# Performance work log

Measured on AMD Instinct MI355X. Metric: run time of the kernel, lower is better.

The kernel has to match this reference:

```python
import jax, jax.numpy as jnp
import numpy as np

# dims: d_model D, d_inner DI=2*D, d_state S, dt_rank R, conv kernel K, layers NL
D, DI, S, R, K, NL = 512, 1024, 16, 32, 4, 6
B, L = 4, 1024
EPS = 1e-5


def _ln(x, w, b):
    m = x.mean(-1, keepdims=True)
    v = ((x - m) ** 2).mean(-1, keepdims=True)
    return (x - m) * jax.lax.rsqrt(v + EPS) * w + b


def _causal_conv(x, w, b):
    # depthwise causal conv1d: x [B,L,DI], w [DI,K], left-pad K-1 (matches Conv1d(padding=K-1) then crop)
    xp = jnp.pad(x, ((0, 0), (K - 1, 0), (0, 0)))
    y = sum(xp[:, k:k + x.shape[1], :] * w[:, k] for k in range(K))
    return y + b


def _mamba(h, in_w, cw, cb, xp_w, dt_w, dt_b, A_log, Dp, out_w):
    # h: [B,L,D]
    xz = jnp.einsum('bld,ed->ble', h, in_w)        # [B,L,2*DI]
    x, z = jnp.split(xz, 2, axis=-1)
    x = jax.nn.silu(_causal_conv(x, cw, cb))       # [B,L,DI]
    dbc = jnp.einsum('bld,ed->ble', x, xp_w)       # [B,L,R+2S]
    dt_r, Bm, Cm = dbc[..., :R], dbc[..., R:R + S], dbc[..., R + S:]
    dt = jax.nn.softplus(jnp.einsum('blr,dr->bld', dt_r, dt_w) + dt_b)  # [B,L,DI]
    A = -jnp.exp(A_log)                            # [DI,S]

    def step(hst, inp):
        dt_t, B_t, C_t, x_t = inp                  # [B,DI],[B,S],[B,S],[B,DI]
        dA = jnp.exp(dt_t[..., None] * A)          # [B,DI,S]
        hst = dA * hst + (dt_t * x_t)[..., None] * B_t[:, None, :]
        y = jnp.einsum('bds,bs->bd', hst, C_t)
        return hst, y

    h0 = jnp.zeros((x.shape[0], DI, S), x.dtype)
    xs = (dt.transpose(1, 0, 2), Bm.transpose(1, 0, 2), Cm.transpose(1, 0, 2), x.transpose(1, 0, 2))
    _, ys = jax.lax.scan(step, h0, xs)
    y = ys.transpose(1, 0, 2) + x * Dp
    y = y * jax.nn.silu(z)
    return jnp.einsum('bld,ed->ble', y, out_w)     # [B,L,D]


def setup_inputs() -> dict:
    key = jax.random.key(0)
    ks = jax.random.split(key, 10)
    n = lambda k, shp, s: s * jax.random.normal(k, shp, jnp.float32)
    inp = {}
    inp['xs_pad'] = jax.random.normal(ks[0], (B, L, D), jnp.float32)
    inp['ilens'] = jax.random.randint(ks[1], (B,), 1, L + 1)
    inp['norm_w'] = jnp.ones((NL, D), jnp.float32)
    inp['norm_b'] = jnp.zeros((NL, D), jnp.float32)
    inp['in_proj_w'] = n(ks[2], (NL, 2 * DI, D), 0.02)
    inp['conv_w'] = n(ks[3], (NL, DI, K), 0.1)
    inp['conv_b'] = jnp.zeros((NL, DI), jnp.float32)
    inp['x_proj_w'] = n(ks[4], (NL, R + 2 * S, DI), 0.02)
    inp['dt_proj_w'] = n(ks[5], (NL, DI, R), 0.1)
    inp['dt_proj_b'] = n(ks[6], (NL, DI), 0.01)
    inp['A_log'] = jnp.log(jnp.broadcast_to(jnp.arange(1, S + 1, dtype=jnp.float32), (NL, DI, S)))
    inp['D_param'] = jnp.ones((NL, DI), jnp.float32)
    inp['out_proj_w'] = n(ks[7], (NL, D, DI), 0.02)
    inp['normf_w'] = jnp.ones((D,), jnp.float32)
    inp['normf_b'] = jnp.zeros((D,), jnp.float32)
    inp['after_w'] = jnp.ones((D,), jnp.float32)
    inp['after_b'] = jnp.zeros((D,), jnp.float32)
    return inp


def reference(xs_pad, ilens, norm_w, norm_b, in_proj_w, conv_w, conv_b, x_proj_w,
              dt_proj_w, dt_proj_b, A_log, D_param, out_proj_w,
              normf_w, normf_b, after_w, after_b):
    hidden = xs_pad
    residual = None
    for i in range(NL):
        residual = hidden + residual if residual is not None else hidden
        hn = _ln(residual, norm_w[i], norm_b[i])
        hidden = _mamba(hn, in_proj_w[i], conv_w[i], conv_b[i], x_proj_w[i],
                        dt_proj_w[i], dt_proj_b[i], A_log[i], D_param[i], out_proj_w[i])
    residual = hidden + residual
    out = _ln(residual, normf_w, normf_b)   # norm_f
    out = _ln(out, after_w, after_b)        # after_norm (normalize_before=True)
    olens = jnp.minimum(ilens, L)
    return out, olens
```

## Files before the change

### kernel.cpp

```cpp
#include <hip/hip_runtime.h>
#include <hip/hip_bf16.h>
#include <math.h>

#define D_   512
#define DI_  1024
#define S_   16
#define R_   32
#define KC_  4
#define NL_  6
#define B_   4
#define L_   1024
#define BL_  (B_*L_)
#define NC_  64
#define CL_  (L_/NC_)
#define BDI_ (B_*DI_)
#define LOG2E 1.44269504f
#define SKX  8
#define SKO  4

typedef __hip_bfloat16 bf16;
typedef __attribute__((ext_vector_type(8))) short bf16x8;
typedef __attribute__((ext_vector_type(4))) float f32x4;
typedef unsigned short u16;

#define QIDX(s, c, bd) (((size_t)(s) * NC_ + (c)) * BDI_ + (bd))

__device__ __forceinline__ float b2f(u16 u) {
  union { unsigned int i; float f; } x; x.i = ((unsigned int)u) << 16; return x.f;
}

__device__ __forceinline__ float softplus_f(float v) {
  float e = __expf(-fabsf(v));
  return fmaxf(v, 0.f) + __logf(1.f + e);
}

__device__ __forceinline__ void gload16(const void* g, void* l) {
  __builtin_amdgcn_global_load_lds((const __attribute__((address_space(1))) void*)g,
                                   (__attribute__((address_space(3))) void*)l, 16, 0, 0);
}

#define N1_ (NL_*2*DI_*D_)
#define N2_ (N1_ + NL_*D_*DI_)
#define N3_ (N2_ + NL_*128*DI_)
#define N4_ (N3_ + NL_*DI_)
__global__ void setup_k(const float* __restrict__ in_w, const float* __restrict__ out_w,
                        const float* __restrict__ xp_w, const float* __restrict__ A_log,
                        bf16* __restrict__ inw_b, bf16* __restrict__ outw_b,
                        bf16* __restrict__ xpw_b,
                        float* __restrict__ an2b, float* __restrict__ ff,
                        float* __restrict__ an2f) {
  for (int i = blockIdx.x * blockDim.x + threadIdx.x; i < N4_; i += gridDim.x * blockDim.x) {
    if (i < N1_) {
      inw_b[i] = __float2bfloat16(in_w[i]);
    } else if (i < N2_) {
      int j = i - N1_;
      outw_b[j] = __float2bfloat16(out_w[j]);
    } else if (i < N3_) {
      int j = i - N2_;
      int c = j & (DI_ - 1);
      int r = (j >> 10) & 127;
      int l = j >> 17;
      float v = (r < 64) ? xp_w[((size_t)l * 64 + r) * DI_ + c] : 0.f;
      xpw_b[j] = __float2bfloat16(v);
    } else {
      int j = i - N3_;
      int d = j & (DI_ - 1);
      int l = j >> 10;
      float base = -expf(A_log[(size_t)j * S_]) * LOG2E;
      bool fast = true;
      #pragma unroll
      for (int s = 0; s < S_; ++s) {
        float a = -expf(A_log[(size_t)j * S_ + s]) * LOG2E;
        an2f[((size_t)l * S_ + s) * DI_ + d] = a;
        fast = fast && (fabsf(a - (float)(s + 1) * base) <= 1e-5f * fabsf(a));
      }
      an2b[j] = base;
      ff[j] = fast ? 1.f : 0.f;
    }
  }
}

__global__ __launch_bounds__(128) void addln_k(
    const float* __restrict__ x0, const u16* __restrict__ parts,
    float* __restrict__ resid, const float* __restrict__ w, const float* __restrict__ b,
    bf16* __restrict__ hn, int first)
{
  __shared__ float red[4];
  const int row = blockIdx.x, t = threadIdx.x;
  const int lane = t & 63, wv = t >> 6;
  float4 v;
  if (first) {
    v = *(const float4*)(x0 + (size_t)row * D_ + t * 4);
  } else {
    const size_t ps = (size_t)BL_ * D_;
    const size_t o = (size_t)row * D_ + t * 4;
    v.x = 0.f; v.y = 0.f; v.z = 0.f; v.w = 0.f;
    #pragma unroll
    for (int p = 0; p < SKO; ++p) {
      ushort4 q = *(const ushort4*)(parts + p * ps + o);
      v.x += b2f(q.x); v.y += b2f(q.y); v.z += b2f(q.z); v.w += b2f(q.w);
    }
    float4 r = *(const float4*)(resid + o);
    v.x += r.x; v.y += r.y; v.z += r.z; v.w += r.w;
  }
  *(float4*)(resid + (size_t)row * D_ + t * 4) = v;
  float s = v.x + v.y + v.z + v.w;
  float ss = v.x*v.x + v.y*v.y + v.z*v.z + v.w*v.w;
  #pragma unroll
  for (int o = 32; o > 0; o >>= 1) { s += __shfl_xor(s, o); ss += __shfl_xor(ss, o); }
  if (lane == 0) { red[wv * 2] = s; red[wv * 2 + 1] = ss; }
  __syncthreads();
  float S = red[0] + red[2], SS = red[1] + red[3];
  float m = S * (1.f / D_), var = SS * (1.f / D_) - m * m;
  float rs = rsqrtf(var + 1e-5f);
  float4 w4 = *(const float4*)(w + t * 4);
  float4 b4 = *(const float4*)(b + t * 4);
  bf16* o = hn + (size_t)row * D_ + t * 4;
  o[0] = __float2bfloat16((v.x - m) * rs * w4.x + b4.x);
  o[1] = __float2bfloat16((v.y - m) * rs * w4.y + b4.y);
  o[2] = __float2bfloat16((v.z - m) * rs * w4.z + b4.z);
  o[3] = __float2bfloat16((v.w - m) * rs * w4.w + b4.w);
}

__global__ __launch_bounds__(256) void gemm_bt(
    const bf16* __restrict__ A, int lda,
    const bf16* __restrict__ B, int ldb,
    bf16* __restrict__ Cb,
    int K, int Nact, int M, int epi)
{
  __shared__ __align__(16) bf16 As[128 * 32];
  __shared__ __align__(16) bf16 Bs[128 * 32];
  const int tid = threadIdx.x;
  const int wave = tid >> 6, lane = tid & 63;
  const int bm = blockIdx.x * 128, bn = blockIdx.y * 128;
  const int kz = blockIdx.z;
  const int Kc = K / gridDim.z;
  const int k0 = kz * Kc, k1 = k0 + Kc;
  const int wr = (wave >> 1) << 6, wc = (wave & 1) << 6;
  const int srow = lane >> 2, scg = lane & 3;
  const int rA = lane & 15, kq = (lane >> 4) << 3;
  f32x4 acc[4][4] = {};
  for (int kt = k0; kt < k1; kt += 32) {
    __syncthreads();
    #pragma unroll
    for (int p = 0; p < 2; ++p) {
      int chunk = wave * 2 + p;
      int row = (chunk << 4) + srow;
      gload16(A + (size_t)(bm + row) * lda + kt + scg * 8, &As[chunk * 512]);
      gload16(B + (size_t)(bn + row) * ldb + kt + scg * 8, &Bs[chunk * 512]);
    }
    __syncthreads();
    bf16x8 af[4], bq[4];
    #pragma unroll
    for (int m = 0; m < 4; ++m) af[m] = *(const bf16x8*)&As[(wr + m * 16 + rA) * 32 + kq];
    #pragma unroll
    for (int n = 0; n < 4; ++n) bq[n] = *(const bf16x8*)&Bs[(wc + n * 16 + rA) * 32 + kq];
    #pragma unroll
    for (int m = 0; m < 4; ++m)
      #pragma unroll
      for (int n = 0; n < 4; ++n)
        acc[m][n] = __builtin_amdgcn_mfma_f32_16x16x32_bf16(af[m], bq[n], acc[m][n], 0, 0, 0);
  }
  const int cr = (lane >> 4) << 2, cc = lane & 15;
  const size_t pbase = (epi == 1) ? (size_t)kz * M * Nact : 0;
  #pragma unroll
  for (int m = 0; m < 4; ++m)
    #pragma unroll
    for (int n = 0; n < 4; ++n) {
      int col = bn + wc + n * 16 + cc;
      if (col >= Nact) continue;
      #pragma unroll
      for (int j = 0; j < 4; ++j) {
        size_t row = (size_t)(bm + wr + m * 16 + cr + j);
        Cb[pbase + row * Nact + col] = __float2bfloat16(acc[m][n][j]);
      }
    }
}

__global__ __launch_bounds__(256) void redx_k(
    const u16* __restrict__ part, float* __restrict__ dbc)
{
  int i = blockIdx.x * 256 + threadIdx.x;
  const size_t ps = (size_t)BL_ * 64;
  float v = 0.f;
  #pragma unroll
  for (int p = 0; p < SKX; ++p) v += b2f(part[p * ps + i]);
  dbc[i] = v;
}

__global__ __launch_bounds__(256) void conv_silu_k(
    const u16* __restrict__ xz, const float* __restrict__ cw, const float* __restrict__ cb,
    bf16* __restrict__ xcb)
{
  int g = blockIdx.x * 256 + threadIdx.x;
  int dq = g & (DI_ / 8 - 1);
  int bl = g >> 7;
  int l = bl & (L_ - 1), b = bl >> 10;
  int d = dq * 8;
  float a[8], wv[8][KC_];
  #pragma unroll
  for (int e = 0; e < 8; ++e) {
    float4 w4 = *(const float4*)(cw + (d + e) * KC_);
    wv[e][0] = w4.x; wv[e][1] = w4.y; wv[e][2] = w4.z; wv[e][3] = w4.w;
    a[e] = cb[d + e];
  }
  #pragma unroll
  for (int k = 0; k < KC_; ++k) {
    int lt = l + k - 3;
    if (lt < 0) continue;
    bf16x8 xv = *(const bf16x8*)(xz + (size_t)(b * L_ + lt) * (2 * DI_) + d);
    #pragma unroll
    for (int e = 0; e < 8; ++e) a[e] += b2f((u16)xv[e]) * wv[e][k];
  }
  bf16 o8[8];
  #pragma unroll
  for (int e = 0; e < 8; ++e) {
    float v = a[e] / (1.f + __expf(-a[e]));
    o8[e] = __float2bfloat16(v);
  }
  *(bf16x8*)(xcb + (size_t)bl * DI_ + d) = *(const bf16x8*)o8;
}


__global__ __launch_bounds__(256) void scanA_k(
    const u16* __restrict__ x, const float* __restrict__ dbc,
    const float* __restrict__ dtw, const float* __restrict__ dtbias,
    const float* __restrict__ A_log, const float* __restrict__ an2b,
    const float* __restrict__ ff, float* __restrict__ sumdt,
    bf16* __restrict__ q, bf16* __restrict__ dtb)
{
  __shared__ float BS[CL_ * 16];
  __shared__ float DTR[CL_ * 32];
  const int tid = threadIdx.x;
  int g = blockIdx.x * 256 + tid;
  int d = g & (DI_ - 1);
  int cb = g >> 10;
  int b = cb & (B_ - 1);
  int c = cb >> 2;
  {
    int step = tid >> 4, off = tid & 15;
    BS[tid] = dbc[((size_t)(b * L_ + c * CL_ + step)) * 64 + R_ + off];
    int f = tid * 2;
    int st2 = f >> 5, of2 = f & 31;
    float2 v = *(const float2*)(dbc + ((size_t)(b * L_ + c * CL_ + st2)) * 64 + of2);
    DTR[f] = v.x; DTR[f + 1] = v.y;
  }
  float wv[R_];
  #pragma unroll
  for (int r = 0; r < R_; r += 4) {
    float4 w4 = *(const float4*)(dtw + (size_t)d * R_ + r);
    wv[r] = w4.x; wv[r + 1] = w4.y; wv[r + 2] = w4.z; wv[r + 3] = w4.w;
  }
  const float bias = dtbias[d];
  const float An2b = an2b[d];
  const bool fast = (ff[d] != 0.f);
  __syncthreads();
  float h[S_] = {};
  float sdt = 0.f;
  const size_t base = ((size_t)b * L_ + c * CL_) * DI_ + d;
  float cx = b2f(x[base]);
  float dtv;
  {
    float v = bias;
    #pragma unroll
    for (int r = 0; r < R_; r += 4) {
      float4 dv = *(const float4*)&DTR[r];
      v += dv.x * wv[r] + dv.y * wv[r + 1] + dv.z * wv[r + 2] + dv.w * wv[r + 3];
    }
    dtv = softplus_f(v);
  }
  for (int i = 0; i < CL_; ++i) {
    const int ip = (i + 1 < CL_) ? i + 1 : i;
    float nx = b2f(x[base + (size_t)ip * DI_]);
    float vn = bias;
    #pragma unroll
    for (int r = 0; r < R_; r += 4) {
      float4 dv = *(const float4*)&DTR[ip * 32 + r];
      vn += dv.x * wv[r] + dv.y * wv[r + 1] + dv.z * wv[r + 2] + dv.w * wv[r + 3];
    }
    dtb[base + (size_t)i * DI_] = __float2bfloat16(dtv);
    sdt += dtv;
    float u = dtv * cx;
    float Bv[S_];
    *(float4*)&Bv[0]  = *(const float4*)&BS[i * 16 + 0];
    *(float4*)&Bv[4]  = *(const float4*)&BS[i * 16 + 4];
    *(float4*)&Bv[8]  = *(const float4*)&BS[i * 16 + 8];
    *(float4*)&Bv[12] = *(const float4*)&BS[i * 16 + 12];
    float da[S_];
    if (fast) {
      float E1 = exp2f(dtv * An2b);
      float E2 = E1 * E1;
      float E4 = E2 * E2;
      da[0] = E1; da[1] = E2; da[2] = E2 * E1; da[3] = E4;
      #pragma unroll
      for (int s = 4; s < S_; ++s) da[s] = da[s - 4] * E4;
    } else {
      #pragma unroll
      for (int s = 0; s < S_; ++s)
        da[s] = exp2f(dtv * (-expf(A_log[(size_t)d * S_ + s]) * LOG2E));
    }
    #pragma unroll
    for (int s = 0; s < S_; ++s) h[s] = da[s] * h[s] + u * Bv[s];
    dtv = softplus_f(vn);
    cx = nx;
  }
  int bd = b * DI_ + d;
  sumdt[(size_t)c * BDI_ + bd] = sdt;
  #pragma unroll
  for (int s = 0; s < S_; ++s) q[QIDX(s, c, bd)] = __float2bfloat16(h[s]);
}

__global__ __launch_bounds__(256) void scanB_k(
    const float* __restrict__ sumdt, const u16* __restrict__ q,
    const float* __restrict__ an2f, bf16* __restrict__ hi)
{
  int g = blockIdx.x * 256 + threadIdx.x;
  int s = g >> 12;
  int bd = g & (BDI_ - 1);
  int d = bd & (DI_ - 1);
  float An2 = an2f[(size_t)s * DI_ + d];
  float h = 0.f;
  float sd = sumdt[bd];
  float qq = b2f(q[(size_t)s * NC_ * BDI_ + bd]);
  for (int c = 0; c < NC_; ++c) {
    float sdn = sd, qn = qq;
    if (c + 1 < NC_) {
      sdn = sumdt[(size_t)(c + 1) * BDI_ + bd];
      qn  = b2f(q[QIDX(s, c + 1, bd)]);
    }
    hi[QIDX(s, c, bd)] = __float2bfloat16(h);
    h = exp2f(An2 * sd) * h + qq;
    sd = sdn; qq = qn;
  }
}

__global__ __launch_bounds__(256) void scanC_k(
    const u16* __restrict__ dt, const u16* __restrict__ x, const float* __restrict__ dbc,
    const float* __restrict__ A_log, const float* __restrict__ an2b,
    const float* __restrict__ ff, const float* __restrict__ Dp, const u16* __restrict__ xz,
    const u16* __restrict__ hi, bf16* __restrict__ y)
{
  __shared__ float BCS[CL_ * 32];
  const int tid = threadIdx.x;
  int g = blockIdx.x * 256 + tid;
  int d = g & (DI_ - 1);
  int cb = g >> 10;
  int b = cb & (B_ - 1);
  int c = cb >> 2;
  {
    int f = tid * 2;
    int step = f >> 5, off = f & 31;
    float2 v = *(const float2*)(dbc + ((size_t)(b * L_ + c * CL_ + step)) * 64 + R_ + off);
    BCS[f] = v.x; BCS[f + 1] = v.y;
  }
  const float An2b = an2b[d];
  const bool fast = (ff[d] != 0.f);
  int bd = b * DI_ + d;
  float h[S_];
  #pragma unroll
  for (int s = 0; s < S_; ++s) h[s] = b2f(hi[QIDX(s, c, bd)]);
  __syncthreads();
  float dpv = Dp[d];
  const size_t rid0 = (size_t)b * L_ + c * CL_;
  const size_t base = rid0 * DI_ + d;
  float cdt = b2f(dt[base]), cx = b2f(x[base]);
  float cz = b2f(xz[rid0 * (2 * DI_) + DI_ + d]);
  float Ecur = exp2f(cdt * An2b);
  for (int i = 0; i < CL_; ++i) {
    const int ip = (i + 1 < CL_) ? i + 1 : i;
    float ndt = b2f(dt[base + (size_t)ip * DI_]);
    float nx  = b2f(x[base + (size_t)ip * DI_]);
    float nz  = b2f(xz[(rid0 + ip) * (2 * DI_) + DI_ + d]);
    float Enext = exp2f(ndt * An2b);
    float u = cdt * cx;
    float Bv[S_], Cv[S_];
    *(float4*)&Bv[0]  = *(const float4*)&BCS[i * 32 + 0];
    *(float4*)&Bv[4]  = *(const float4*)&BCS[i * 32 + 4];
    *(float4*)&Bv[8]  = *(const float4*)&BCS[i * 32 + 8];
    *(float4*)&Bv[12] = *(const float4*)&BCS[i * 32 + 12];
    *(float4*)&Cv[0]  = *(const float4*)&BCS[i * 32 + 16];
    *(float4*)&Cv[4]  = *(const float4*)&BCS[i * 32 + 20];
    *(float4*)&Cv[8]  = *(const float4*)&BCS[i * 32 + 24];
    *(float4*)&Cv[12] = *(const float4*)&BCS[i * 32 + 28];
    float da[S_];
    if (fast) {
      float E1 = Ecur;
      float E2 = E1 * E1;
      float E4 = E2 * E2;
      da[0] = E1; da[1] = E2; da[2] = E2 * E1; da[3] = E4;
      #pragma unroll
      for (int s = 4; s < S_; ++s) da[s] = da[s - 4] * E4;
    } else {
      #pragma unroll
      for (int s = 0; s < S_; ++s)
        da[s] = exp2f(cdt * (-expf(A_log[(size_t)d * S_ + s]) * LOG2E));
    }
    float acc = 0.f;
    #pragma unroll
    for (int s = 0; s < S_; ++s) {
      h[s] = da[s] * h[s] + u * Bv[s];
      acc += h[s] * Cv[s];
    }
    acc += cx * dpv;
    acc *= cz / (1.f + __expf(-cz));
    y[(rid0 + i) * DI_ + d] = __float2bfloat16(acc);
    cdt = ndt; cx = nx; cz = nz; Ecur = Enext;
  }
}

__global__ __launch_bounds__(128) void final_k(
    const u16* __restrict__ parts, const float* __restrict__ res,
    const float* __restrict__ fw, const float* __restrict__ fb,
    const float* __restrict__ aw, const float* __restrict__ ab,
    const int* __restrict__ ilens, float* __restrict__ out, int outN)
{
  __shared__ float red[4];
  const int row = blockIdx.x, t = threadIdx.x;
  const int lane = t & 63, wv = t >> 6;
  const size_t ps = (size_t)BL_ * D_;
  const size_t o0 = (size_t)row * D_ + t * 4;
  float4 v; v.x = 0.f; v.y = 0.f; v.z = 0.f; v.w = 0.f;
  #pragma unroll
  for (int p = 0; p < SKO; ++p) {
    ushort4 q = *(const ushort4*)(parts + p * ps + o0);
    v.x += b2f(q.x); v.y += b2f(q.y); v.z += b2f(q.z); v.w += b2f(q.w);
  }
  float4 r = *(const float4*)(res + o0);
  v.x += r.x; v.y += r.y; v.z += r.z; v.w += r.w;
  float s = v.x + v.y + v.z + v.w;
  float ss = v.x*v.x + v.y*v.y + v.z*v.z + v.w*v.w;
  #pragma unroll
  for (int o = 32; o > 0; o >>= 1) { s += __shfl_xor(s, o); ss += __shfl_xor(ss, o); }
  if (lane == 0) { red[wv * 2] = s; red[wv * 2 + 1] = ss; }
  __syncthreads();
  float S = red[0] + red[2], SS = red[1] + red[3];
  float m = S * (1.f / D_), var = SS * (1.f / D_) - m * m;
  float rs = rsqrtf(var + 1e-5f);
  float4 w4 = *(const float4*)(fw + t * 4);
  float4 b4 = *(const float4*)(fb + t * 4);
  float4 x1;
  x1.x = (v.x - m) * rs * w4.x + b4.x;
  x1.y = (v.y - m) * rs * w4.y + b4.y;
  x1.z = (v.z - m) * rs * w4.z + b4.z;
  x1.w = (v.w - m) * rs * w4.w + b4.w;
  __syncthreads();
  float s2 = x1.x + x1.y + x1.z + x1.w;
  float ss2 = x1.x*x1.x + x1.y*x1.y + x1.z*x1.z + x1.w*x1.w;
  #pragma unroll
  for (int o = 32; o > 0; o >>= 1) { s2 += __shfl_xor(s2, o); ss2 += __shfl_xor(ss2, o); }
  if (lane == 0) { red[wv * 2] = s2; red[wv * 2 + 1] = ss2; }
  __syncthreads();
  float S2 = red[0] + red[2], SS2 = red[1] + red[3];
  float m2 = S2 * (1.f / D_), var2 = SS2 * (1.f / D_) - m2 * m2;
  float rs2 = rsqrtf(var2 + 1e-5f);
  float4 aw4 = *(const float4*)(aw + t * 4);
  float4 ab4 = *(const float4*)(ab + t * 4);
  float4 o;
  o.x = (x1.x - m2) * rs2 * aw4.x + ab4.x;
  o.y = (x1.y - m2) * rs2 * aw4.y + ab4.y;
  o.z = (x1.z - m2) * rs2 * aw4.z + ab4.z;
  o.w = (x1.w - m2) * rs2 * aw4.w + ab4.w;
  *(float4*)(out + (size_t)row * D_ + t * 4) = o;
  if (row == 0 && t < B_) {
    int q = ilens[t];
    out[outN + t] = (float)(q < L_ ? q : L_);
  }
}

extern "C" void kernel_launch(void* const* d_in, const int* in_sizes, int n_in,
                              void* d_out, int out_size, void* d_ws, size_t ws_size,
                              hipStream_t stream) {
  const float* xs     = (const float*)d_in[0];
  const int*   ilens  = (const int*)d_in[1];
  const float* norm_w = (const float*)d_in[2];
  const float* norm_b = (const float*)d_in[3];
  const float* in_w   = (const float*)d_in[4];
  const float* conv_w = (const float*)d_in[5];
  const float* conv_b = (const float*)d_in[6];
  const float* xp_w   = (const float*)d_in[7];
  const float* dt_w   = (const float*)d_in[8];
  const float* dt_b   = (const float*)d_in[9];
  const float* A_log  = (const float*)d_in[10];
  const float* Dp     = (const float*)d_in[11];
  const float* out_w  = (const float*)d_in[12];
  const float* nfw    = (const float*)d_in[13];
  const float* nfb    = (const float*)d_in[14];
  const float* afw    = (const float*)d_in[15];
  const float* afb    = (const float*)d_in[16];
  float* out = (float*)d_out;

  char* ws = (char*)d_ws;
  size_t off = 0;
  auto alloc = [&](size_t bytes) -> char* {
    char* p = ws + off;
    off += (bytes + 255) & ~(size_t)255;
    return p;
  };
  bf16*  inw_b  = (bf16*)alloc((size_t)NL_ * 2 * DI_ * D_ * 2);
  bf16*  outw_b = (bf16*)alloc((size_t)NL_ * D_ * DI_ * 2);
  bf16*  xpw_b  = (bf16*)alloc((size_t)NL_ * 128 * DI_ * 2);
  float* an2b   = (float*)alloc((size_t)NL_ * DI_ * 4);
  float* ffb    = (float*)alloc((size_t)NL_ * DI_ * 4);
  float* an2f   = (float*)alloc((size_t)NL_ * S_ * DI_ * 4);
  float* resid  = (float*)alloc((size_t)BL_ * D_ * 4);
  bf16*  hn_b   = (bf16*)alloc((size_t)BL_ * D_ * 2);
  bf16*  xzb    = (bf16*)alloc((size_t)BL_ * 2 * DI_ * 2);
  bf16*  xcb    = (bf16*)alloc((size_t)BL_ * DI_ * 2);
  bf16*  xpart  = (bf16*)alloc((size_t)SKX * BL_ * 64 * 2);
  float* dbc    = (float*)alloc((size_t)BL_ * 64 * 4);
  bf16*  dtb    = (bf16*)alloc((size_t)BL_ * DI_ * 2);
  float* sdt    = (float*)alloc((size_t)NC_ * BDI_ * 4);
  bf16*  qb     = (bf16*)alloc((size_t)S_ * NC_ * BDI_ * 2);
  bf16*  hini   = (bf16*)alloc((size_t)S_ * NC_ * BDI_ * 2);
  bf16*  yb     = (bf16*)alloc((size_t)BL_ * DI_ * 2);
  bf16*  opart  = (bf16*)alloc((size_t)SKO * BL_ * D_ * 2);
  if (off > ws_size) return;

  setup_k<<<4096, 256, 0, stream>>>(in_w, out_w, xp_w, A_log,
                                    inw_b, outw_b, xpw_b, an2b, ffb, an2f);

  for (int i = 0; i < NL_; ++i) {
    addln_k<<<BL_, 128, 0, stream>>>(xs, (const u16*)opart, resid,
                                     norm_w + i * D_, norm_b + i * D_, hn_b, i == 0);
    dim3 g1(32, 16, 1);
    gemm_bt<<<g1, 256, 0, stream>>>(hn_b, D_, inw_b + (size_t)i * 2 * DI_ * D_, D_,
                                    xzb, D_, 2 * DI_, BL_, 3);
    conv_silu_k<<<(BL_ * DI_ / 8) / 256, 256, 0, stream>>>(
        (const u16*)xzb, conv_w + i * DI_ * KC_, conv_b + i * DI_, xcb);
    dim3 g2(32, 1, SKX);
    gemm_bt<<<g2, 256, 0, stream>>>(xcb, DI_, xpw_b + (size_t)i * 128 * DI_, DI_,
                                    xpart, DI_, 64, BL_, 1);
    redx_k<<<(BL_ * 64) / 256, 256, 0, stream>>>((const u16*)xpart, dbc);
    scanA_k<<<(NC_ * B_ * DI_) / 256, 256, 0, stream>>>(
        (const u16*)xcb, dbc, dt_w + (size_t)i * DI_ * R_, dt_b + i * DI_,
        A_log + (size_t)i * DI_ * S_, an2b + i * DI_, ffb + i * DI_, sdt, qb, dtb);
    scanB_k<<<(B_ * DI_ * S_) / 256, 256, 0, stream>>>(
        sdt, (const u16*)qb, an2f + (size_t)i * S_ * DI_, hini);
    scanC_k<<<(NC_ * B_ * DI_) / 256, 256, 0, stream>>>(
        (const u16*)dtb, (const u16*)xcb, dbc, A_log + (size_t)i * DI_ * S_,
        an2b + i * DI_, ffb + i * DI_, Dp + i * DI_,
        (const u16*)xzb, (const u16*)hini, yb);
    dim3 g4(32, 4, SKO);
    gemm_bt<<<g4, 256, 0, stream>>>(yb, DI_, outw_b + (size_t)i * D_ * DI_, DI_,
                                    opart, DI_, D_, BL_, 1);
  }
  final_k<<<BL_, 128, 0, stream>>>((const u16*)opart, resid, nfw, nfb, afw, afb, ilens, out,
                                   out_size - B_);
}
```

Measured before the change: 724.0 us.

## Move dt projection out of scanA into a bf16 MFMA GEMM with softplus epilogue

The dt_proj matmul plus bias and softplus is no longer computed with scalar FMAs inside scanA_k. It now runs as a separate MFMA GEMM over a bf16 copy of the x_proj output, with bias and softplus applied in the GEMM epilogue. scanA_k then just reads the precomputed bf16 dt. This strips a 32-wide dot product per step from the scan's inner loop, but adds a kernel launch and an extra round trip of dt through memory. It also quantizes dt_r and dt_w to bf16.

Measured after the change: 794.2 us. 1.1x slower.

```diff
diff --git a/kernel.cpp b/kernel.cpp
--- a/kernel.cpp
+++ b/kernel.cpp
@@ -39,14 +39,16 @@
                                    (__attribute__((address_space(3))) void*)l, 16, 0, 0);
 }
 
-#define N1_ (NL_*2*DI_*D_)
-#define N2_ (N1_ + NL_*D_*DI_)
-#define N3_ (N2_ + NL_*128*DI_)
-#define N4_ (N3_ + NL_*DI_)
+#define N1_  (NL_*2*DI_*D_)
+#define N2_  (N1_ + NL_*D_*DI_)
+#define N3_  (N2_ + NL_*128*DI_)
+#define N3B_ (N3_ + NL_*DI_*R_)
+#define N4_  (N3B_ + NL_*DI_)
 __global__ void setup_k(const float* __restrict__ in_w, const float* __restrict__ out_w,
-                        const float* __restrict__ xp_w, const float* __restrict__ A_log,
+                        const float* __restrict__ xp_w, const float* __restrict__ dt_w,
+                        const float* __restrict__ A_log,
                         bf16* __restrict__ inw_b, bf16* __restrict__ outw_b,
-                        bf16* __restrict__ xpw_b,
+                        bf16* __restrict__ xpw_b, bf16* __restrict__ dtw_b,
                         float* __restrict__ an2b, float* __restrict__ ff,
                         float* __restrict__ an2f) {
   for (int i = blockIdx.x * blockDim.x + threadIdx.x; i < N4_; i += gridDim.x * blockDim.x) {
@@ -62,8 +64,11 @@
       int l = j >> 17;
       float v = (r < 64) ? xp_w[((size_t)l * 64 + r) * DI_ + c] : 0.f;
       xpw_b[j] = __float2bfloat16(v);
+    } else if (i < N3B_) {
+      int j = i - N3_;
+      dtw_b[j] = __float2bfloat16(dt_w[j]);
     } else {
-      int j = i - N3_;
+      int j = i - N3B_;
       int d = j & (DI_ - 1);
       int l = j >> 10;
       float base = -expf(A_log[(size_t)j * S_]) * LOG2E;
@@ -125,7 +130,7 @@
 __global__ __launch_bounds__(256) void gemm_bt(
     const bf16* __restrict__ A, int lda,
     const bf16* __restrict__ B, int ldb,
-    bf16* __restrict__ Cb,
+    bf16* __restrict__ Cb, const float* __restrict__ bias,
     int K, int Nact, int M, int epi)
 {
   __shared__ __align__(16) bf16 As[128 * 32];
@@ -172,13 +177,15 @@
       #pragma unroll
       for (int j = 0; j < 4; ++j) {
         size_t row = (size_t)(bm + wr + m * 16 + cr + j);
-        Cb[pbase + row * Nact + col] = __float2bfloat16(acc[m][n][j]);
+        float v = acc[m][n][j];
+        if (epi == 2) v = softplus_f(v + bias[col]);
+        Cb[pbase + row * Nact + col] = __float2bfloat16(v);
       }
     }
 }
 
 __global__ __launch_bounds__(256) void redx_k(
-    const u16* __restrict__ part, float* __restrict__ dbc)
+    const u16* __restrict__ part, float* __restrict__ dbc, bf16* __restrict__ dbcb)
 {
   int i = blockIdx.x * 256 + threadIdx.x;
   const size_t ps = (size_t)BL_ * 64;
@@ -186,6 +193,7 @@
   #pragma unroll
   for (int p = 0; p < SKX; ++p) v += b2f(part[p * ps + i]);
   dbc[i] = v;
+  dbcb[i] = __float2bfloat16(v);
 }
 
 __global__ __launch_bounds__(256) void conv_silu_k(
@@ -223,14 +231,12 @@
 
 
 __global__ __launch_bounds__(256) void scanA_k(
-    const u16* __restrict__ x, const float* __restrict__ dbc,
-    const float* __restrict__ dtw, const float* __restrict__ dtbias,
-    const float* __restrict__ A_log, const float* __restrict__ an2b,
-    const float* __restrict__ ff, float* __restrict__ sumdt,
-    bf16* __restrict__ q, bf16* __restrict__ dtb)
+    const u16* __restrict__ dt, const u16* __restrict__ x, const float* __restrict__ dbc,
+    const float* __restrict__ an2b, const float* __restrict__ ff,
+    const float* __restrict__ A_log,
+    float* __restrict__ sumdt, bf16* __restrict__ q)
 {
   __shared__ float BS[CL_ * 16];
-  __shared__ float DTR[CL_ * 32];
   const int tid = threadIdx.x;
   int g = blockIdx.x * 256 + tid;
   int d = g & (DI_ - 1);
@@ -240,47 +246,20 @@
   {
     int step = tid >> 4, off = tid & 15;
     BS[tid] = dbc[((size_t)(b * L_ + c * CL_ + step)) * 64 + R_ + off];
-    int f = tid * 2;
-    int st2 = f >> 5, of2 = f & 31;
-    float2 v = *(const float2*)(dbc + ((size_t)(b * L_ + c * CL_ + st2)) * 64 + of2);
-    DTR[f] = v.x; DTR[f + 1] = v.y;
-  }
-  float wv[R_];
-  #pragma unroll
-  for (int r = 0; r < R_; r += 4) {
-    float4 w4 = *(const float4*)(dtw + (size_t)d * R_ + r);
-    wv[r] = w4.x; wv[r + 1] = w4.y; wv[r + 2] = w4.z; wv[r + 3] = w4.w;
-  }
-  const float bias = dtbias[d];
+  }
   const float An2b = an2b[d];
   const bool fast = (ff[d] != 0.f);
   __syncthreads();
   float h[S_] = {};
   float sdt = 0.f;
   const size_t base = ((size_t)b * L_ + c * CL_) * DI_ + d;
-  float cx = b2f(x[base]);
-  float dtv;
-  {
-    float v = bias;
-    #pragma unroll
-    for (int r = 0; r < R_; r += 4) {
-      float4 dv = *(const float4*)&DTR[r];
-      v += dv.x * wv[r] + dv.y * wv[r + 1] + dv.z * wv[r + 2] + dv.w * wv[r + 3];
-    }
-    dtv = softplus_f(v);
-  }
+  float cdt = b2f(dt[base]), cx = b2f(x[base]);
   for (int i = 0; i < CL_; ++i) {
     const int ip = (i + 1 < CL_) ? i + 1 : i;
-    float nx = b2f(x[base + (size_t)ip * DI_]);
-    float vn = bias;
-    #pragma unroll
-    for (int r = 0; r < R_; r += 4) {
-      float4 dv = *(const float4*)&DTR[ip * 32 + r];
-      vn += dv.x * wv[r] + dv.y * wv[r + 1] + dv.z * wv[r + 2] + dv.w * wv[r + 3];
-    }
-    dtb[base + (size_t)i * DI_] = __float2bfloat16(dtv);
-    sdt += dtv;
-    float u = dtv * cx;
+    float ndt = b2f(dt[base + (size_t)ip * DI_]);
+    float nx  = b2f(x[base + (size_t)ip * DI_]);
+    float u = cdt * cx;
+    sdt += cdt;
     float Bv[S_];
     *(float4*)&Bv[0]  = *(const float4*)&BS[i * 16 + 0];
     *(float4*)&Bv[4]  = *(const float4*)&BS[i * 16 + 4];
@@ -288,7 +267,7 @@
     *(float4*)&Bv[12] = *(const float4*)&BS[i * 16 + 12];
     float da[S_];
     if (fast) {
-      float E1 = exp2f(dtv * An2b);
+      float E1 = exp2f(cdt * An2b);
       float E2 = E1 * E1;
       float E4 = E2 * E2;
       da[0] = E1; da[1] = E2; da[2] = E2 * E1; da[3] = E4;
@@ -297,12 +276,11 @@
     } else {
       #pragma unroll
       for (int s = 0; s < S_; ++s)
-        da[s] = exp2f(dtv * (-expf(A_log[(size_t)d * S_ + s]) * LOG2E));
+        da[s] = exp2f(cdt * (-expf(A_log[(size_t)d * S_ + s]) * LOG2E));
     }
     #pragma unroll
     for (int s = 0; s < S_; ++s) h[s] = da[s] * h[s] + u * Bv[s];
-    dtv = softplus_f(vn);
-    cx = nx;
+    cdt = ndt; cx = nx;
   }
   int bd = b * DI_ + d;
   sumdt[(size_t)c * BDI_ + bd] = sdt;
@@ -499,6 +477,7 @@
   bf16*  inw_b  = (bf16*)alloc((size_t)NL_ * 2 * DI_ * D_ * 2);
   bf16*  outw_b = (bf16*)alloc((size_t)NL_ * D_ * DI_ * 2);
   bf16*  xpw_b  = (bf16*)alloc((size_t)NL_ * 128 * DI_ * 2);
+  bf16*  dtw_b  = (bf16*)alloc((size_t)NL_ * DI_ * R_ * 2);
   float* an2b   = (float*)alloc((size_t)NL_ * DI_ * 4);
   float* ffb    = (float*)alloc((size_t)NL_ * DI_ * 4);
   float* an2f   = (float*)alloc((size_t)NL_ * S_ * DI_ * 4);
@@ -508,6 +487,7 @@
   bf16*  xcb    = (bf16*)alloc((size_t)BL_ * DI_ * 2);
   bf16*  xpart  = (bf16*)alloc((size_t)SKX * BL_ * 64 * 2);
   float* dbc    = (float*)alloc((size_t)BL_ * 64 * 4);
+  bf16*  dbcb   = (bf16*)alloc((size_t)BL_ * 64 * 2);
   bf16*  dtb    = (bf16*)alloc((size_t)BL_ * DI_ * 2);
   float* sdt    = (float*)alloc((size_t)NC_ * BDI_ * 4);
   bf16*  qb     = (bf16*)alloc((size_t)S_ * NC_ * BDI_ * 2);
@@ -516,24 +496,27 @@
   bf16*  opart  = (bf16*)alloc((size_t)SKO * BL_ * D_ * 2);
   if (off > ws_size) return;
 
-  setup_k<<<4096, 256, 0, stream>>>(in_w, out_w, xp_w, A_log,
-                                    inw_b, outw_b, xpw_b, an2b, ffb, an2f);
+  setup_k<<<4096, 256, 0, stream>>>(in_w, out_w, xp_w, dt_w, A_log,
+                                    inw_b, outw_b, xpw_b, dtw_b, an2b, ffb, an2f);
 
   for (int i = 0; i < NL_; ++i) {
     addln_k<<<BL_, 128, 0, stream>>>(xs, (const u16*)opart, resid,
                                      norm_w + i * D_, norm_b + i * D_, hn_b, i == 0);
     dim3 g1(32, 16, 1);
     gemm_bt<<<g1, 256, 0, stream>>>(hn_b, D_, inw_b + (size_t)i * 2 * DI_ * D_, D_,
-                                    xzb, D_, 2 * DI_, BL_, 3);
+                                    xzb, nullptr, D_, 2 * DI_, BL_, 3);
     conv_silu_k<<<(BL_ * DI_ / 8) / 256, 256, 0, stream>>>(
         (const u16*)xzb, conv_w + i * DI_ * KC_, conv_b + i * DI_, xcb);
     dim3 g2(32, 1, SKX);
     gemm_bt<<<g2, 256, 0, stream>>>(xcb, DI_, xpw_b + (size_t)i * 128 * DI_, DI_,
-                                    xpart, DI_, 64, BL_, 1);
-    redx_k<<<(BL_ * 64) / 256, 256, 0, stream>>>((const u16*)xpart, dbc);
+                                    xpart, nullptr, DI_, 64, BL_, 1);
+    redx_k<<<(BL_ * 64) / 256, 256, 0, stream>>>((const u16*)xpart, dbc, dbcb);
+    dim3 g3(32, 8, 1);
+    gemm_bt<<<g3, 256, 0, stream>>>(dbcb, 64, dtw_b + (size_t)i * DI_ * R_, R_,
+                                    dtb, dt_b + i * DI_, R_, DI_, BL_, 2);
     scanA_k<<<(NC_ * B_ * DI_) / 256, 256, 0, stream>>>(
-        (const u16*)xcb, dbc, dt_w + (size_t)i * DI_ * R_, dt_b + i * DI_,
-        A_log + (size_t)i * DI_ * S_, an2b + i * DI_, ffb + i * DI_, sdt, qb, dtb);
+        (const u16*)dtb, (const u16*)xcb, dbc,
+        an2b + i * DI_, ffb + i * DI_, A_log + (size_t)i * DI_ * S_, sdt, qb);
     scanB_k<<<(B_ * DI_ * S_) / 256, 256, 0, stream>>>(
         sdt, (const u16*)qb, an2f + (size_t)i * S_ * DI_, hini);
     scanC_k<<<(NC_ * B_ * DI_) / 256, 256, 0, stream>>>(
@@ -542,7 +525,7 @@
         (const u16*)xzb, (const u16*)hini, yb);
     dim3 g4(32, 4, SKO);
     gemm_bt<<<g4, 256, 0, stream>>>(yb, DI_, outw_b + (size_t)i * D_ * DI_, DI_,
-                                    opart, DI_, D_, BL_, 1);
+                                    opart, nullptr, DI_, D_, BL_, 1);
   }
   final_k<<<BL_, 128, 0, stream>>>((const u16*)opart, resid, nfw, nfb, afw, afb, ilens, out,
                                    out_size - B_);
```
